# Performance work log

Measured on AMD Instinct MI355X. Metric: run time of the kernel, lower is better.

## Reference

```python
import jax, jax.numpy as jnp
import numpy as np

D = 512; N = 1536; H = 4; DH = D // H
MAX_INT = 5; BINS = 100; LAYERS = 3


def _mha(q_in, k_in, v_in, in_w, in_b, out_w, out_b):
    """PyTorch-style nn.MultiheadAttention (batch of 1). Returns (out [Nq,D], head-avg weights [Nq,Nk])."""
    wq, wk, wv = in_w[:D], in_w[D:2 * D], in_w[2 * D:]
    bq, bk, bv = in_b[:D], in_b[D:2 * D], in_b[2 * D:]
    n_q, n_k = q_in.shape[0], k_in.shape[0]
    q = (q_in @ wq.T + bq).reshape(n_q, H, DH).transpose(1, 0, 2)  # [H,Nq,dh]
    k = (k_in @ wk.T + bk).reshape(n_k, H, DH).transpose(1, 0, 2)
    v = (v_in @ wv.T + bv).reshape(n_k, H, DH).transpose(1, 0, 2)
    scores = jnp.einsum('hqd,hkd->hqk', q, k) / jnp.sqrt(jnp.asarray(DH, q.dtype))
    w = jax.nn.softmax(scores, axis=-1)  # [H,Nq,Nk]
    out = jnp.einsum('hqk,hkd->hqd', w, v).transpose(1, 0, 2).reshape(n_q, D)
    out = out @ out_w.T + out_b
    return out, w.mean(0)


def setup_inputs() -> dict:
    key = jax.random.key(0)
    ks = jax.random.split(key, 12)
    s = 0.02
    return {
        'node_embeddings': jax.random.normal(ks[0], (N, D), jnp.float32),
        'time_positions': jax.random.uniform(ks[1], (N, 1), jnp.float32) * 10.0,
        'batch_indices': jnp.zeros((N,), jnp.int32),
        'W_time': jax.random.normal(ks[2], (D, 1), jnp.float32) * s,
        'b_time': jnp.zeros((D,), jnp.float32),
        'in_w': jax.random.normal(ks[3], (3 * D, D), jnp.float32) * s,
        'in_b': jnp.zeros((3 * D,), jnp.float32),
        'out_w': jax.random.normal(ks[4], (D, D), jnp.float32) * s,
        'out_b': jnp.zeros((D,), jnp.float32),
        'ic_w1': jax.random.normal(ks[5], (128, D), jnp.float32) * s,
        'ic_b1': jnp.zeros((128,), jnp.float32),
        'ic_w2': jax.random.normal(ks[6], (MAX_INT, 128), jnp.float32) * s,
        'ic_b2': jnp.zeros((MAX_INT,), jnp.float32),
        'ref_w1': jax.random.normal(ks[7], (LAYERS, 128, D + 2), jnp.float32) * s,
        'ref_b1': jnp.zeros((LAYERS, 128), jnp.float32),
        'ref_w2': jax.random.normal(ks[8], (LAYERS, 2 * BINS, 128), jnp.float32) * s,
        'ref_b2': jnp.zeros((LAYERS, 2 * BINS), jnp.float32),
        'weight_params': jnp.linspace(-0.5, 0.5, BINS).astype(jnp.float32),
        'qp_w': jax.random.normal(ks[9], (D, D + 2), jnp.float32) * s,
        'qp_b': jnp.zeros((D,), jnp.float32),
    }


def _forward(node_embeddings, time_positions, W_time, b_time, in_w, in_b, out_w, out_b,
             ic_w1, ic_b1, ic_w2, ic_b2, ref_w1, ref_b1, ref_w2, ref_b2,
             weight_params, qp_w, qp_b):
    x = node_embeddings + time_positions @ W_time.T + b_time  # [N,D]
    attn_out, _ = _mha(x, x, x, in_w, in_b, out_w, out_b)      # [N,D]
    pooled = attn_out.mean(0)                                   # [D]
    probs = jax.nn.softmax(ic_w2 @ jax.nn.relu(ic_w1 @ pooled + ic_b1) + ic_b2)
    num_intervals = jnp.argmax(probs) + 1
    interval_mask = jnp.arange(MAX_INT) < num_intervals
    t_min, t_max = time_positions.min(), time_positions.max()
    grid = jnp.linspace(t_min, t_max, MAX_INT + 1)
    start, end = grid[:-1], grid[1:]                            # [MAX_INT]
    n = attn_out.shape[0]
    ones = jnp.ones((n, 1), attn_out.dtype)

    def per_interval(s_i, e_i, w1, b1, w2, b2):
        query = jnp.concatenate([attn_out, ones * s_i, ones * e_i], axis=-1)  # [N,D+2]
        qp = query @ qp_w.T + qp_b                                            # [N,D]
        h = jax.nn.relu(query @ w1.T + b1)
        logits = h @ w2.T + b2                                                # [N,2*BINS]
        s_off = (jax.nn.softmax(logits[:, :BINS], axis=-1) * weight_params).sum(-1)  # [N]
        e_off = (jax.nn.softmax(logits[:, BINS:], axis=-1) * weight_params).sum(-1)
        _, aw = _mha(qp, attn_out, attn_out, in_w, in_b, out_w, out_b)        # [N,N]
        return (aw * s_off).sum(), (aw * e_off).sum()

    for l in range(LAYERS):  # layers have distinct params; intervals are independent within a layer
        ds, de = jax.vmap(per_interval, in_axes=(0, 0, None, None, None, None))(
            start, end, ref_w1[l], ref_b1[l], ref_w2[l], ref_b2[l])
        start = start + ds
        end = end + de

    final_bounds = jnp.stack([start, end], axis=-1)  # [MAX_INT,2]
    return final_bounds, interval_mask


def reference(node_embeddings, time_positions, batch_indices, W_time, b_time, in_w, in_b,
              out_w, out_b, ic_w1, ic_b1, ic_w2, ic_b2, ref_w1, ref_b1, ref_w2, ref_b2,
              weight_params, qp_w, qp_b):
    return _forward(node_embeddings, time_positions, W_time, b_time, in_w, in_b, out_w, out_b,
                    ic_w1, ic_b1, ic_w2, ic_b2, ref_w1, ref_b1, ref_w2, ref_b2,
                    weight_params, qp_w, qp_b)
```

## Files before the change

kernel.cpp:

```cpp
#include <hip/hip_runtime.h>
#include <hip/hip_bf16.h>

typedef __hip_bfloat16 bf16;
typedef __bf16 bf16x8 __attribute__((ext_vector_type(8)));
typedef float f32x4 __attribute__((ext_vector_type(4)));

#define DD   512
#define NT   1536
#define NH   4
#define DHD  128
#define NBINS 100
#define MAXI 5
#define NL   3
#define RSQRT_DH 0.08838834764831845f

#define OFF_ATT    ((size_t)0)
#define OFF_CTX    (OFF_ATT  + (size_t)NT*DD)
#define OFF_CTX1   (OFF_CTX  + (size_t)NT*DD)
#define OFF_H0     (OFF_CTX1 + (size_t)NT*DD)
#define OFF_LG     (OFF_H0   + (size_t)NT*384)
#define OFF_AARR   (OFF_LG   + (size_t)8*NH*NT*16)
#define OFF_BARR   (OFF_AARR + (size_t)NH*NT)
#define OFF_AV     (OFF_BARR + (size_t)NH*NT)
#define OFF_BV     (OFF_AV   + (size_t)DD)
#define OFF_B2     (OFF_BV   + (size_t)DD)
#define OFF_SOFF   (OFF_B2   + (size_t)DD)
#define OFF_EOFF   (OFF_SOFF + (size_t)MAXI*NT)
#define OFF_STAT   (OFF_EOFF + (size_t)MAXI*NT)
#define OFF_POOL   (OFF_STAT + (size_t)NH*NT*12)
#define OFF_SCAL   (OFF_POOL + (size_t)DD)
#define OFF_E      (OFF_SCAL + (size_t)64)
#define SC_START 0
#define SC_END   5
#define SC_DSDE  10
#define SC_CNT   20
#define PSLICE   ((size_t)NH*NT*16)
#define BF_BASE  (OFF_E + (size_t)NH*NT*NT/2)
#define BQKB   ((size_t)0)
#define BVT    (BQKB  + (size_t)NT*1024)
#define BATT   (BVT   + (size_t)NH*128*NT)
#define BK2    (BATT  + (size_t)NT*512)
#define BQ0    (BK2   + (size_t)NT*512)
#define BM2    (BQ0   + (size_t)NT*512)
#define BINW   (BM2   + (size_t)512*512)
#define BOUTW  (BINW  + (size_t)1536*512)
#define BRW1   (BOUTW + (size_t)512*512)
#define BRW2   (BRW1  + (size_t)384*512)

__device__ __forceinline__ void cvt8(const float* s, bf16* d) {
    float4 f0 = *(const float4*)s, f1 = *(const float4*)(s + 4);
    union { uint4 u; unsigned short us[8]; } o;
    bf16 t;
    t = __float2bfloat16(f0.x); o.us[0] = *(unsigned short*)&t;
    t = __float2bfloat16(f0.y); o.us[1] = *(unsigned short*)&t;
    t = __float2bfloat16(f0.z); o.us[2] = *(unsigned short*)&t;
    t = __float2bfloat16(f0.w); o.us[3] = *(unsigned short*)&t;
    t = __float2bfloat16(f1.x); o.us[4] = *(unsigned short*)&t;
    t = __float2bfloat16(f1.y); o.us[5] = *(unsigned short*)&t;
    t = __float2bfloat16(f1.z); o.us[6] = *(unsigned short*)&t;
// ... 115 lines not shown
        for (int it = 0; it < 32; it++) {
            size_t g = start + it * 256 + tid;
            cvt8(out_w + g * 8, bp + BOUTW + g * 8);
        }
    } else if (bx < 97) {
        size_t start = (size_t)(bx - 93) * 6144;
        for (int it = 0; it < 24; it++) {
            size_t g = start + it * 256 + tid;
            int row = (int)(g >> 6), col = (int)(g & 63) * 8;
            const float* s = ref_w1 + (size_t)row * 514 + col;
            float buf[8];
#pragma unroll
            for (int q = 0; q < 4; q++) { float2 f = *(const float2*)(s + 2 * q); buf[2 * q] = f.x; buf[2 * q + 1] = f.y; }
            cvt8(buf, bp + BRW1 + (size_t)row * 512 + col);
        }
    } else {
        for (int it = 0; it < 38; it++) {
            size_t g = (size_t)it * 256 + tid;
            if (g < 9600) cvt8(ref_w2 + g * 8, bp + BRW2 + g * 8);
        }
    }
}

template <int STATS>
__global__ __launch_bounds__(256) void k_score(
    const bf16* __restrict__ Ab, int lda, int aZ,
    const bf16* __restrict__ Bb, int ldb, int bZ,
    bf16* __restrict__ E, float* __restrict__ stat)
{
    int z = blockIdx.z;
    const __bf16* A = (const __bf16*)Ab + (size_t)z * aZ;
    const __bf16* B = (const __bf16*)Bb + (size_t)z * bZ;
    int m0 = blockIdx.y * 128, n0 = blockIdx.x * 128;
    __shared__ __bf16 As[128 * 40];
    __shared__ __bf16 Bs[128 * 40];
    __shared__ float sSum[4][64];
    int tid = threadIdx.x;
    int r = tid >> 1, hh = tid & 1;
    int w = tid >> 6, lane = tid & 63;
    int wm = (w & 1) * 64, wn = (w >> 1) * 64;
    int lr = lane & 15, lq = lane >> 4;
    f32x4 acc[4][4];
#pragma unroll
    for (int i = 0; i < 4; i++)
#pragma unroll
        for (int j = 0; j < 4; j++) acc[i][j] = (f32x4){0.f, 0.f, 0.f, 0.f};

    const __bf16* arow = A + (size_t)(m0 + r) * lda + hh * 16;
    const __bf16* brow = B + (size_t)(n0 + r) * ldb + hh * 16;
    __bf16* awr = &As[r * 40 + hh * 16];
    __bf16* bwr = &Bs[r * 40 + hh * 16];

    for (int k0 = 0; k0 < DHD; k0 += 32) {
        uint4 a0 = *(const uint4*)(arow + k0);
        uint4 a1 = *(const uint4*)(arow + k0 + 8);
        uint4 b0 = *(const uint4*)(brow + k0);
        uint4 b1 = *(const uint4*)(brow + k0 + 8);
        __syncthreads();
        *(uint4*)awr = a0; *(uint4*)(awr + 8) = a1;
        *(uint4*)bwr = b0; *(uint4*)(bwr + 8) = b1;
        __syncthreads();
        bf16x8 af[4], bfr[4];
#pragma unroll
        for (int i = 0; i < 4; i++) af[i] = *(bf16x8*)&As[(wm + i * 16 + lr) * 40 + lq * 8];
#pragma unroll
        for (int j = 0; j < 4; j++) bfr[j] = *(bf16x8*)&Bs[(wn + j * 16 + lr) * 40 + lq * 8];
#pragma unroll
        for (int i = 0; i < 4; i++)
#pragma unroll
            for (int j = 0; j < 4; j++)
                acc[i][j] = __builtin_amdgcn_mfma_f32_16x16x32_bf16(af[i], bfr[j], acc[i][j], 0, 0, 0);
    }
    bf16* Ez = E + (size_t)z * NT * NT;
#pragma unroll
    for (int i = 0; i < 4; i++)
#pragma unroll
        for (int r4 = 0; r4 < 4; r4++) {
            int gm = m0 + wm + i * 16 + lq * 4 + r4;
            float s = 0.f;
#pragma unroll
            for (int j = 0; j < 4; j++) {
                float e = __expf(acc[i][j][r4] * RSQRT_DH);
                Ez[(size_t)gm * NT + n0 + wn + j * 16 + lr] = __float2bfloat16(e);
                s += e;
            }
            if (STATS) {
                for (int off = 1; off < 16; off <<= 1) s += __shfl_xor(s, off);
                if (lr == 0) sSum[w][i * 16 + lq * 4 + r4] = s;
            }
        }
    if (STATS) {
        __syncthreads();
        if (tid < 128) {
            int lidx = tid & 63, wb = tid >> 6;
            stat[((size_t)z * NT + m0 + tid) * 12 + blockIdx.x] = sSum[wb][lidx] + sSum[wb + 2][lidx];
        }
    }
}

__global__ __launch_bounds__(256) void k_qkv(
    const float* __restrict__ emb, const float* __restrict__ t,
    const float* __restrict__ wt, const float* __restrict__ bt,
    const float* __restrict__ in_b, float* ws)
{
    bf16* bp = (bf16*)(ws + BF_BASE);
    int m0 = blockIdx.y * 64, n0 = blockIdx.x * 64;
    __shared__ __bf16 As[64 * 40];
    __shared__ __bf16 Bs[64 * 40];
    int tid = threadIdx.x;
    int r = tid >> 2, quad = tid & 3;
    int w = tid >> 6, lane = tid & 63;
    int wm = (w & 1) * 32, wn = (w >> 1) * 32;
    int lr = lane & 15, lq = lane >> 4;
    f32x4 acc[2][2];
#pragma unroll
    for (int i = 0; i < 2; i++)
#pragma unroll
        for (int j = 0; j < 2; j++) acc[i][j] = (f32x4){0.f, 0.f, 0.f, 0.f};

    float trow = t[m0 + r];
    const float* arow = emb + (size_t)(m0 + r) * DD + quad * 8;
    const __bf16* brow = (const __bf16*)(bp + BINW) + (size_t)(n0 + r) * 512 + quad * 8;
// ... 31 lines not shown
#pragma unroll
    for (int i = 0; i < 2; i++)
#pragma unroll
        for (int j = 0; j < 2; j++) {
            int gn = n0 + wn + j * 16 + lr;
            int gmb = m0 + wm + i * 16 + lq * 4;
            float b = in_b[gn];
            if (gn < 2 * DD) {
#pragma unroll
                for (int r4 = 0; r4 < 4; r4++)
                    QKB[(size_t)(gmb + r4) * 1024 + gn] = __float2bfloat16(acc[i][j][r4] + b);
            } else {
                union { uint2 u; unsigned short us[4]; } o;
#pragma unroll
                for (int r4 = 0; r4 < 4; r4++) {
                    bf16 t2 = __float2bfloat16(acc[i][j][r4] + b);
                    o.us[r4] = *(unsigned short*)&t2;
                }
                *(uint2*)&VtB[(size_t)(gn - 2 * DD) * NT + gmb] = o.u;
            }
        }
}

__global__ __launch_bounds__(256) void k_pv(const bf16* __restrict__ E, float* ws) {
    bf16* bp = (bf16*)(ws + BF_BASE);
    int h = blockIdx.z;
    int m0 = blockIdx.y * 64;
    int ks = blockIdx.x;
    const int KCH = NT / 2;
    int kbeg = ks * KCH;
    __shared__ __bf16 As[64 * 40];
    __shared__ __bf16 Bs[128 * 40];
    __shared__ float sI[64];
    int tid = threadIdx.x;
    if (tid < 64) {
        const float* st = ws + OFF_STAT + (size_t)(h * NT + m0 + tid) * 12;
        float den = 0.f;
#pragma unroll
        for (int t2 = 0; t2 < 12; t2++) den += st[t2];
        sI[tid] = 1.f / den;
    }
    int rA = tid >> 2, quadA = tid & 3;
    int rB = tid >> 1, hhB = tid & 1;
    int w = tid >> 6, lane = tid & 63;
    int wm = (w & 1) * 32, wn = (w >> 1) * 64;
    int lr = lane & 15, lq = lane >> 4;
    const __bf16* Eh = (const __bf16*)E + (size_t)h * NT * NT;
    const __bf16* arow = Eh + (size_t)(m0 + rA) * NT + quadA * 8;
    const __bf16* brow = (const __bf16*)(bp + BVT) + ((size_t)h * 128 + rB) * NT + hhB * 16;
    __bf16* awr = &As[rA * 40 + quadA * 8];
    __bf16* bwr = &Bs[rB * 40 + hhB * 16];
    f32x4 acc[2][4];
#pragma unroll
    for (int i = 0; i < 2; i++)
#pragma unroll
        for (int j = 0; j < 4; j++) acc[i][j] = (f32x4){0.f, 0.f, 0.f, 0.f};

    for (int k0 = kbeg; k0 < kbeg + KCH; k0 += 32) {
        uint4 av = *(const uint4*)(arow + k0);
        uint4 b0 = *(const uint4*)(brow + k0);
        uint4 b1 = *(const uint4*)(brow + k0 + 8);
        __syncthreads();
        *(uint4*)awr = av;
        *(uint4*)bwr = b0; *(uint4*)(bwr + 8) = b1;
        __syncthreads();
        bf16x8 af[2], bfr[4];
#pragma unroll
        for (int i = 0; i < 2; i++) af[i] = *(bf16x8*)&As[(wm + i * 16 + lr) * 40 + lq * 8];
#pragma unroll
        for (int j = 0; j < 4; j++) bfr[j] = *(bf16x8*)&Bs[(wn + j * 16 + lr) * 40 + lq * 8];
#pragma unroll
        for (int i = 0; i < 2; i++)
#pragma unroll
            for (int j = 0; j < 4; j++)
                acc[i][j] = __builtin_amdgcn_mfma_f32_16x16x32_bf16(af[i], bfr[j], acc[i][j], 0, 0, 0);
    }
    float* dst = ws + (ks == 0 ? OFF_CTX : OFF_CTX1);
#pragma unroll
    for (int i = 0; i < 2; i++)
#pragma unroll
        for (int r4 = 0; r4 < 4; r4++) {
            int lrow = wm + i * 16 + lq * 4 + r4;
            float ri = sI[lrow];
#pragma unroll
            for (int j = 0; j < 4; j++) {
                int gn = wn + j * 16 + lr;
                dst[(size_t)(m0 + lrow) * DD + h * DHD + gn] = acc[i][j][r4] * ri;
            }
        }
}

__global__ __launch_bounds__(256) void k_oproj(const float* __restrict__ out_b, float* ws) {
    bf16* bp = (bf16*)(ws + BF_BASE);
    int m0 = blockIdx.y * 64, n0 = blockIdx.x * 64;
    __shared__ __bf16 As[64 * 40];
    __shared__ __bf16 Bs[64 * 40];
    __shared__ float ps[64];
    int tid = threadIdx.x;
    int r = tid >> 2, quad = tid & 3;
    int w = tid >> 6, lane = tid & 63;
    int wm = (w & 1) * 32, wn = (w >> 1) * 32;
    int lr = lane & 15, lq = lane >> 4;
    f32x4 acc[2][2];
#pragma unroll
    for (int i = 0; i < 2; i++)
#pragma unroll
        for (int j = 0; j < 2; j++) acc[i][j] = (f32x4){0.f, 0.f, 0.f, 0.f};
    if (tid < 64) ps[tid] = 0.f;

    const float* a0 = ws + OFF_CTX  + (size_t)(m0 + r) * DD + quad * 8;
    const float* a1 = ws + OFF_CTX1 + (size_t)(m0 + r) * DD + quad * 8;
    const __bf16* brow = (const __bf16*)(bp + BOUTW) + (size_t)(n0 + r) * 512 + quad * 8;
    __bf16* awr = &As[r * 40 + quad * 8];
    __bf16* bwr = &Bs[r * 40 + quad * 8];

    for (int k0 = 0; k0 < DD; k0 += 32) {
        __bf16 ta[8] __attribute__((aligned(16)));
#pragma unroll
        for (int q = 0; q < 4; q++) {
            float2 x = *(const float2*)(a0 + k0 + 2 * q);
            float2 y = *(const float2*)(a1 + k0 + 2 * q);
            ta[2 * q]     = (__bf16)(x.x + y.x);
            ta[2 * q + 1] = (__bf16)(x.y + y.y);
        }
        uint4 bbv = *(const uint4*)(brow + k0);
        __syncthreads();
        *(bf16x8*)awr = *(bf16x8*)ta;
        *(uint4*)bwr = bbv;
        __syncthreads();
        bf16x8 af[2], bfr[2];
#pragma unroll
        for (int i = 0; i < 2; i++) af[i] = *(bf16x8*)&As[(wm + i * 16 + lr) * 40 + lq * 8];
#pragma unroll
        for (int j = 0; j < 2; j++) bfr[j] = *(bf16x8*)&Bs[(wn + j * 16 + lr) * 40 + lq * 8];
#pragma unroll
        for (int i = 0; i < 2; i++)
#pragma unroll
            for (int j = 0; j < 2; j++)
                acc[i][j] = __builtin_amdgcn_mfma_f32_16x16x32_bf16(af[i], bfr[j], acc[i][j], 0, 0, 0);
    }
    float* att = ws + OFF_ATT;
    bf16* attB = bp + BATT;
#pragma unroll
    for (int j = 0; j < 2; j++) {
        int gn = n0 + wn + j * 16 + lr;
        float b = out_b[gn];
// ... 38 lines not shown
            float4 a = *(const float4*)wr, b = *(const float4*)(wr + 4);
            float d = a.x * p8[0] + a.y * p8[1] + a.z * p8[2] + a.w * p8[3]
                    + b.x * p8[4] + b.y * p8[5] + b.z * p8[6] + b.w * p8[7];
            for (int off = 32; off; off >>= 1) d += __shfl_xor(d, off);
            if (lane == 0) h1[row] = fmaxf(d * (1.0f / NT) + icb1[row], 0.f);
        }
        __syncthreads();
        if (tid < MAXI) {
            float s = icb2[tid];
            for (int j = 0; j < 128; j++) s += icw2[tid * 128 + j] * h1[j];
            lg[tid] = s;
        }
        __syncthreads();
        if (tid == 0) {
            int best = 0; float bv = lg[0];
            for (int m = 1; m < MAXI; m++) if (lg[m] > bv) { bv = lg[m]; best = m; }
            int ni = best + 1;
            for (int i = 0; i < MAXI; i++) out[10 + i] = (i < ni) ? 1.f : 0.f;
        }
        return;
    }
    const __bf16* B; const float* bias; int n0, mode;
    bf16* Cb = nullptr; float* Cf = nullptr;
    if (bx < 8)       { B = (const __bf16*)(bp + BINW) + (size_t)512 * 512; bias = in_b + DD;     Cb = bp + BK2; n0 = bx * 64; mode = 0; }
    else if (bx < 16) { B = (const __bf16*)(bp + BM2);                      bias = ws + OFF_B2;   Cb = bp + BQ0; n0 = (bx - 8) * 64; mode = 0; }
    else              { B = (const __bf16*)(bp + BRW1);                     bias = ref_b1;        Cf = ws + OFF_H0; n0 = (bx - 16) * 64; mode = 1; }
    int m0 = blockIdx.y * 64;
    int r = tid >> 2, quad = tid & 3;
    int w = tid >> 6, lane = tid & 63;
    int wm = (w & 1) * 32, wn = (w >> 1) * 32;
    int lr = lane & 15, lq = lane >> 4;
    f32x4 acc[2][2];
#pragma unroll
    for (int i = 0; i < 2; i++)
#pragma unroll
        for (int j = 0; j < 2; j++) acc[i][j] = (f32x4){0.f, 0.f, 0.f, 0.f};

    const __bf16* arow = (const __bf16*)(bp + BATT) + (size_t)(m0 + r) * 512 + quad * 8;
    const __bf16* brow = B + (size_t)(n0 + r) * 512 + quad * 8;
    __bf16* awr = &As[r * 40 + quad * 8];
    __bf16* bwr = &Bs[r * 40 + quad * 8];

    for (int k0 = 0; k0 < DD; k0 += 32) {
        uint4 av = *(const uint4*)(arow + k0);
        uint4 bv = *(const uint4*)(brow + k0);
        __syncthreads();
        *(uint4*)awr = av;
        *(uint4*)bwr = bv;
        __syncthreads();
// ... 3 lines not shown
#pragma unroll
        for (int j = 0; j < 2; j++) bfr[j] = *(bf16x8*)&Bs[(wn + j * 16 + lr) * 40 + lq * 8];
#pragma unroll
        for (int i = 0; i < 2; i++)
#pragma unroll
            for (int j = 0; j < 2; j++)
                acc[i][j] = __builtin_amdgcn_mfma_f32_16x16x32_bf16(af[i], bfr[j], acc[i][j], 0, 0, 0);
    }
#pragma unroll
    for (int i = 0; i < 2; i++)
#pragma unroll
        for (int r4 = 0; r4 < 4; r4++) {
            int gm = m0 + wm + i * 16 + lq * 4 + r4;
#pragma unroll
            for (int j = 0; j < 2; j++) {
                int gn = n0 + wn + j * 16 + lr;
                float v = acc[i][j][r4] + bias[gn];
                if (mode == 0) Cb[(size_t)gm * 512 + gn] = __float2bfloat16(v);
                else           Cf[(size_t)gm * 384 + gn] = v;
            }
        }
}

__global__ __launch_bounds__(256) void k_abc(float* ws) {
    bf16* bp = (bf16*)(ws + BF_BASE);
    int wave = threadIdx.x >> 6, lane = threadIdx.x & 63;
    int row = blockIdx.x * 4 + wave;
    int h = row / NT, n = row % NT;
    const unsigned short* k2 = (const unsigned short*)(bp + BK2 + (size_t)n * 512 + h * DHD);
    const float* av = ws + OFF_AV + h * DHD;
    const float* bv = ws + OFF_BV + h * DHD;
    int d = lane * 2;
    float k0 = __uint_as_float((unsigned)k2[d] << 16);
    float k1 = __uint_as_float((unsigned)k2[d + 1] << 16);
    float a = av[d] * k0 + av[d + 1] * k1;
    float b = bv[d] * k0 + bv[d + 1] * k1;
    for (int off = 32; off; off >>= 1) { a += __shfl_xor(a, off); b += __shfl_xor(b, off); }
    if (lane == 0) { ws[OFF_AARR + row] = a * RSQRT_DH; ws[OFF_BARR + row] = b * RSQRT_DH; }
}

__global__ __launch_bounds__(256) void k_lgs(
    const float* __restrict__ rw1, const float* __restrict__ rb2,
    const float* __restrict__ wp, int l, float* ws)
{
    bf16* bp = (bf16*)(ws + BF_BASE);
    __shared__ float dsh[128];
    __shared__ __bf16 As[64 * 136];
    __shared__ __bf16 Bs[64 * 136];
    __shared__ __bf16 Ls[64 * 208];
    int tid = threadIdx.x;
    int m0 = blockIdx.x * 64;
    int i_int = m0 / NT;
    int nbase = m0 % NT;
    if (blockIdx.x == 0 && tid < 11) ws[OFF_SCAL + SC_DSDE + tid] = 0.f;
    if (tid < 128) {
        float s_i = ws[OFF_SCAL + SC_START + i_int], e_i = ws[OFF_SCAL + SC_END + i_int];
        const float* wr = rw1 + (size_t)(l * 128 + tid) * 514;
        dsh[tid] = s_i * wr[512] + e_i * wr[513];
    }
    __syncthreads();
    int r = tid >> 2, quad = tid & 3;
// ... 67 lines not shown
        int c0 = q * 50;
        const unsigned short* lrow = (const unsigned short*)&Ls[rloc * 208];
        float m = -1e30f;
#pragma unroll
        for (int c = 0; c < 50; c++)
            m = fmaxf(m, __uint_as_float((unsigned)lrow[c0 + c] << 16));
        m = fmaxf(m, __shfl_xor(m, 1));
        float den = 0.f, num = 0.f;
#pragma unroll
        for (int c = 0; c < 50; c++) {
            float p = __expf(__uint_as_float((unsigned)lrow[c0 + c] << 16) - m);
            den += p;
            int wc = c0 + c; if (wc >= NBINS) wc -= NBINS;
            num += p * wp[wc];
        }
        den += __shfl_xor(den, 1);
        num += __shfl_xor(num, 1);
        int n = nbase + rloc;
        if (q == 0)      ws[OFF_SOFF + (size_t)i_int * NT + n] = num / den;
        else if (q == 2) ws[OFF_EOFF + (size_t)i_int * NT + n] = num / den;
    }
}

__global__ __launch_bounds__(256) void k_eg(const bf16* __restrict__ E0, float* ws) {
    int h = blockIdx.z;
    int m0 = blockIdx.y * 128;
    int ks = blockIdx.x;
    const int KCH = NT / 8;
    __shared__ __bf16 As[128 * 40];
    __shared__ __bf16 Bs[16 * 40];
    int tid = threadIdx.x;
    int w = tid >> 6, lane = tid & 63;
    int lr = lane & 15, lq = lane >> 4;
    int r = tid >> 1, half = tid & 1;
    const unsigned short* arow =
        (const unsigned short*)((const __bf16*)E0 + (size_t)h * NT * NT + (size_t)(m0 + r) * NT) + half * 16;
    int wm = w * 32;
    f32x4 acc[2];
    acc[0] = (f32x4){0.f, 0.f, 0.f, 0.f};
    acc[1] = (f32x4){0.f, 0.f, 0.f, 0.f};
    int bc = tid >> 3, bk = tid & 7;
    int valid = (tid < 128) && (bc < 15);
    int ii = bc / 3, tt = bc - ii * 3;
    if (ii > 4) ii = 4;
    float s_i = 0.f, e_i = 0.f;
    if (valid) { s_i = ws[OFF_SCAL + SC_START + ii]; e_i = ws[OFF_SCAL + SC_END + ii]; }
    const float* Ar = ws + OFF_AARR + h * NT;
    const float* Br = ws + OFF_BARR + h * NT;
    const float* fo = ws + (tt == 2 ? OFF_EOFF : OFF_SOFF) + (size_t)ii * NT;

    for (int k0 = ks * KCH; k0 < ks * KCH + KCH; k0 += 32) {
        uint4 a0 = *(const uint4*)(arow + k0);
        uint4 a1 = *(const uint4*)(arow + k0 + 8);
        float bv[4] = {0.f, 0.f, 0.f, 0.f};
        if (valid) {
            float4 a4 = *(const float4*)(Ar + k0 + bk * 4);
            float4 b4 = *(const float4*)(Br + k0 + bk * 4);
            bv[0] = __expf(s_i * a4.x + e_i * b4.x);
            bv[1] = __expf(s_i * a4.y + e_i * b4.y);
            bv[2] = __expf(s_i * a4.z + e_i * b4.z);
            bv[3] = __expf(s_i * a4.w + e_i * b4.w);
            if (tt) {
                float4 f4 = *(const float4*)(fo + k0 + bk * 4);
                bv[0] *= f4.x; bv[1] *= f4.y; bv[2] *= f4.z; bv[3] *= f4.w;
            }
        }
        __syncthreads();
        *(uint4*)&As[r * 40 + half * 16] = a0;
        *(uint4*)&As[r * 40 + half * 16 + 8] = a1;
        if (tid < 128) {
            __bf16* bw = &Bs[bc * 40 + bk * 4];
            bw[0] = (__bf16)bv[0]; bw[1] = (__bf16)bv[1]; bw[2] = (__bf16)bv[2]; bw[3] = (__bf16)bv[3];
        }
        __syncthreads();
        bf16x8 bf0 = *(bf16x8*)&Bs[lr * 40 + lq * 8];
        bf16x8 af0 = *(bf16x8*)&As[(wm + lr) * 40 + lq * 8];
        bf16x8 af1 = *(bf16x8*)&As[(wm + 16 + lr) * 40 + lq * 8];
        acc[0] = __builtin_amdgcn_mfma_f32_16x16x32_bf16(af0, bf0, acc[0], 0, 0, 0);
        acc[1] = __builtin_amdgcn_mfma_f32_16x16x32_bf16(af1, bf0, acc[1], 0, 0, 0);
    }
    float* P = ws + OFF_LG + (size_t)ks * PSLICE;
    if (lr < 15) {
#pragma unroll
        for (int i = 0; i < 2; i++)
#pragma unroll
            for (int r4 = 0; r4 < 4; r4++) {
                int gm = m0 + wm + i * 16 + lq * 4 + r4;
                P[(size_t)(h * NT + gm) * 16 + lr] = acc[i][r4];
            }
    }
}

__global__ __launch_bounds__(256) void k_fin(float* ws, float* out, int l) {
    __shared__ float part[4][10];
    int tid = threadIdx.x;
    int w = tid >> 6, lane = tid & 63;
    int row = blockIdx.x * 256 + tid;
    float acc[15];
#pragma unroll
    for (int c = 0; c < 15; c++) acc[c] = 0.f;
    for (int ks = 0; ks < 8; ks++) {
        const float* Pr = ws + OFF_LG + (size_t)ks * PSLICE + (size_t)row * 16;
#pragma unroll
        for (int c = 0; c < 15; c++) acc[c] += Pr[c];
    }
    float loc[10];
#pragma unroll
    for (int i = 0; i < MAXI; i++) {
        float den = acc[i * 3];
        loc[i]        = acc[i * 3 + 1] / den;
        loc[MAXI + i] = acc[i * 3 + 2] / den;
    }
#pragma unroll
    for (int c = 0; c < 10; c++)
        for (int off = 32; off; off >>= 1) loc[c] += __shfl_xor(loc[c], off);
    if (lane == 0) {
#pragma unroll
        for (int c = 0; c < 10; c++) part[w][c] = loc[c];
    }
    __syncthreads();
    if (tid < 10) {
        float s = part[0][tid] + part[1][tid] + part[2][tid] + part[3][tid];
        atomicAdd(&ws[OFF_SCAL + SC_DSDE + tid], s);
    }
    __threadfence();
    __syncthreads();
    if (tid == 0) {
        unsigned old = atomicAdd((unsigned*)&ws[OFF_SCAL + SC_CNT], 1u);
        if (old == 23) {
            for (int i = 0; i < MAXI; i++) {
                float ds = atomicAdd(&ws[OFF_SCAL + SC_DSDE + i], 0.f);
                float de = atomicAdd(&ws[OFF_SCAL + SC_DSDE + MAXI + i], 0.f);
                float ns = ws[OFF_SCAL + SC_START + i] + ds * 0.25f;
                float ne = ws[OFF_SCAL + SC_END + i]   + de * 0.25f;
                ws[OFF_SCAL + SC_START + i] = ns;
                ws[OFF_SCAL + SC_END + i]   = ne;
                if (l == NL - 1) { out[2 * i] = ns; out[2 * i + 1] = ne; }
            }
        }
    }
}

extern "C" void kernel_launch(void* const* d_in, const int* in_sizes, int n_in,
                              void* d_out, int out_size, void* d_ws, size_t ws_size,
                              hipStream_t stream) {
    const float* emb    = (const float*)d_in[0];
    const float* tpos   = (const float*)d_in[1];
    const float* W_time = (const float*)d_in[3];
    const float* b_time = (const float*)d_in[4];
    const float* in_w   = (const float*)d_in[5];
    const float* in_b   = (const float*)d_in[6];
    const float* out_w  = (const float*)d_in[7];
    const float* out_b  = (const float*)d_in[8];
    const float* ic_w1  = (const float*)d_in[9];
    const float* ic_b1  = (const float*)d_in[10];
    const float* ic_w2  = (const float*)d_in[11];
    const float* ic_b2  = (const float*)d_in[12];
    const float* ref_w1 = (const float*)d_in[13];
    const float* ref_b1 = (const float*)d_in[14];
    const float* ref_w2 = (const float*)d_in[15];
    const float* ref_b2 = (const float*)d_in[16];
    const float* wp     = (const float*)d_in[17];
    const float* qp_w   = (const float*)d_in[18];
    const float* qp_b   = (const float*)d_in[19];
    float* ws  = (float*)d_ws;
    float* out = (float*)d_out;
    bf16* E = (bf16*)(ws + OFF_E);
    bf16* bp = (bf16*)(ws + BF_BASE);

    k_misc<<<98, 256, 0, stream>>>(tpos, in_w, in_b, out_w, ref_w1, ref_w2, qp_w, qp_b, ws);

    k_qkv<<<dim3(24, 24), 256, 0, stream>>>(emb, tpos, W_time, b_time, in_b, ws);
    k_score<1><<<dim3(12, 12, NH), 256, 0, stream>>>(
        bp + BQKB, 1024, DHD, bp + BQKB + 512, 1024, DHD, E, ws + OFF_STAT);
    k_pv<<<dim3(2, NT / 64, NH), 256, 0, stream>>>(E, ws);
    k_oproj<<<dim3(8, 24), 256, 0, stream>>>(out_b, ws);

    k_trip<<<dim3(23, 24), 256, 0, stream>>>(in_b, ref_b1, ic_w1, ic_b1, ic_w2, ic_b2, ws, out);

    k_score<0><<<dim3(12, 12, NH), 256, 0, stream>>>(
        bp + BQ0, 512, DHD, bp + BK2, 512, DHD, E, nullptr);
    k_abc<<<NH * NT / 4, 256, 0, stream>>>(ws);

    for (int l = 0; l < NL; l++) {
        k_lgs<<<120, 256, 0, stream>>>(ref_w1, ref_b2 + l * 200, wp, l, ws);
        k_eg<<<dim3(8, NT / 128, NH), 256, 0, stream>>>(E, ws);
        k_fin<<<NH * NT / 256, 256, 0, stream>>>(ws, out, l);
    }
}
```

Before: 305.9 us.

## Fuse first attention into flash-style kernel and merge EG reduction kernels

Replaces the score+PV pair for the first attention with a single fused kernel that computes exp-scores per key tile in shared memory and accumulates context directly, eliminating the materialized E matrix and split-K partials. Folds the k_abc row-dot kernel into an extra z-slice of the second score kernel, and merges the per-layer EG GEMM with its final reduction into one kernel that finalizes via atomics. Reduces launches and global traffic but lowers grid parallelism to 96 blocks for the fused kernels.

Measured after the change: 377.8 us. 1.23x slower.

```diff
diff --git a/kernel.cpp b/kernel.cpp
--- a/kernel.cpp
+++ b/kernel.cpp
@@ -16,25 +16,21 @@
 
 #define OFF_ATT    ((size_t)0)
 #define OFF_CTX    (OFF_ATT  + (size_t)NT*DD)
-#define OFF_CTX1   (OFF_CTX  + (size_t)NT*DD)
-#define OFF_H0     (OFF_CTX1 + (size_t)NT*DD)
-#define OFF_LG     (OFF_H0   + (size_t)NT*384)
-#define OFF_AARR   (OFF_LG   + (size_t)8*NH*NT*16)
+#define OFF_H0     (OFF_CTX  + (size_t)NT*DD)
+#define OFF_AARR   (OFF_H0   + (size_t)NT*384)
 #define OFF_BARR   (OFF_AARR + (size_t)NH*NT)
 #define OFF_AV     (OFF_BARR + (size_t)NH*NT)
 #define OFF_BV     (OFF_AV   + (size_t)DD)
 #define OFF_B2     (OFF_BV   + (size_t)DD)
 #define OFF_SOFF   (OFF_B2   + (size_t)DD)
 #define OFF_EOFF   (OFF_SOFF + (size_t)MAXI*NT)
-#define OFF_STAT   (OFF_EOFF + (size_t)MAXI*NT)
-#define OFF_POOL   (OFF_STAT + (size_t)NH*NT*12)
+#define OFF_POOL   (OFF_EOFF + (size_t)MAXI*NT)
 #define OFF_SCAL   (OFF_POOL + (size_t)DD)
 #define OFF_E      (OFF_SCAL + (size_t)64)
 #define SC_START 0
 #define SC_END   5
 #define SC_DSDE  10
 #define SC_CNT   20
-#define PSLICE   ((size_t)NH*NT*16)
 #define BF_BASE  (OFF_E + (size_t)NH*NT*NT/2)
 #define BQKB   ((size_t)0)
 #define BVT    (BQKB  + (size_t)NT*1024)
@@ -196,82 +192,6 @@
     }
 }
 
-template <int STATS>
-__global__ __launch_bounds__(256) void k_score(
-    const bf16* __restrict__ Ab, int lda, int aZ,
-    const bf16* __restrict__ Bb, int ldb, int bZ,
-    bf16* __restrict__ E, float* __restrict__ stat)
-{
-    int z = blockIdx.z;
-    const __bf16* A = (const __bf16*)Ab + (size_t)z * aZ;
-    const __bf16* B = (const __bf16*)Bb + (size_t)z * bZ;
-    int m0 = blockIdx.y * 128, n0 = blockIdx.x * 128;
-    __shared__ __bf16 As[128 * 40];
-    __shared__ __bf16 Bs[128 * 40];
-    __shared__ float sSum[4][64];
-    int tid = threadIdx.x;
-    int r = tid >> 1, hh = tid & 1;
-    int w = tid >> 6, lane = tid & 63;
-    int wm = (w & 1) * 64, wn = (w >> 1) * 64;
-    int lr = lane & 15, lq = lane >> 4;
-    f32x4 acc[4][4];
-#pragma unroll
-    for (int i = 0; i < 4; i++)
-#pragma unroll
-        for (int j = 0; j < 4; j++) acc[i][j] = (f32x4){0.f, 0.f, 0.f, 0.f};
-
-    const __bf16* arow = A + (size_t)(m0 + r) * lda + hh * 16;
-    const __bf16* brow = B + (size_t)(n0 + r) * ldb + hh * 16;
-    __bf16* awr = &As[r * 40 + hh * 16];
-    __bf16* bwr = &Bs[r * 40 + hh * 16];
-
-    for (int k0 = 0; k0 < DHD; k0 += 32) {
-        uint4 a0 = *(const uint4*)(arow + k0);
-        uint4 a1 = *(const uint4*)(arow + k0 + 8);
-        uint4 b0 = *(const uint4*)(brow + k0);
-        uint4 b1 = *(const uint4*)(brow + k0 + 8);
-        __syncthreads();
-        *(uint4*)awr = a0; *(uint4*)(awr + 8) = a1;
-        *(uint4*)bwr = b0; *(uint4*)(bwr + 8) = b1;
-        __syncthreads();
-        bf16x8 af[4], bfr[4];
-#pragma unroll
-        for (int i = 0; i < 4; i++) af[i] = *(bf16x8*)&As[(wm + i * 16 + lr) * 40 + lq * 8];
-#pragma unroll
-        for (int j = 0; j < 4; j++) bfr[j] = *(bf16x8*)&Bs[(wn + j * 16 + lr) * 40 + lq * 8];
-#pragma unroll
-        for (int i = 0; i < 4; i++)
-#pragma unroll
-            for (int j = 0; j < 4; j++)
-                acc[i][j] = __builtin_amdgcn_mfma_f32_16x16x32_bf16(af[i], bfr[j], acc[i][j], 0, 0, 0);
-    }
-    bf16* Ez = E + (size_t)z * NT * NT;
-#pragma unroll
-    for (int i = 0; i < 4; i++)
-#pragma unroll
-        for (int r4 = 0; r4 < 4; r4++) {
-            int gm = m0 + wm + i * 16 + lq * 4 + r4;
-            float s = 0.f;
-#pragma unroll
-            for (int j = 0; j < 4; j++) {
-                float e = __expf(acc[i][j][r4] * RSQRT_DH);
-                Ez[(size_t)gm * NT + n0 + wn + j * 16 + lr] = __float2bfloat16(e);
-                s += e;
-            }
-            if (STATS) {
-                for (int off = 1; off < 16; off <<= 1) s += __shfl_xor(s, off);
-                if (lr == 0) sSum[w][i * 16 + lq * 4 + r4] = s;
-            }
-        }
-    if (STATS) {
-        __syncthreads();
-        if (tid < 128) {
-            int lidx = tid & 63, wb = tid >> 6;
-            stat[((size_t)z * NT + m0 + tid) * 12 + blockIdx.x] = sSum[wb][lidx] + sSum[wb + 2][lidx];
-        }
-    }
-}
-
 __global__ __launch_bounds__(256) void k_qkv(
     const float* __restrict__ emb, const float* __restrict__ t,
     const float* __restrict__ wt, const float* __restrict__ bt,
@@ -349,71 +269,103 @@
         }
 }
 
-__global__ __launch_bounds__(256) void k_pv(const bf16* __restrict__ E, float* ws) {
+__global__ __launch_bounds__(256) void k_fmha(float* ws) {
     bf16* bp = (bf16*)(ws + BF_BASE);
-    int h = blockIdx.z;
-    int m0 = blockIdx.y * 64;
-    int ks = blockIdx.x;
-    const int KCH = NT / 2;
-    int kbeg = ks * KCH;
-    __shared__ __bf16 As[64 * 40];
-    __shared__ __bf16 Bs[128 * 40];
-    __shared__ float sI[64];
+    int h = blockIdx.y;
+    int m0 = blockIdx.x * 64;
+    __shared__ __bf16 Ks[64 * 136];
+    __shared__ __bf16 Vs[128 * 72];
+    __shared__ __bf16 Es[64 * 72];
     int tid = threadIdx.x;
-    if (tid < 64) {
-        const float* st = ws + OFF_STAT + (size_t)(h * NT + m0 + tid) * 12;
-        float den = 0.f;
-#pragma unroll
-        for (int t2 = 0; t2 < 12; t2++) den += st[t2];
-        sI[tid] = 1.f / den;
-    }
-    int rA = tid >> 2, quadA = tid & 3;
+    int w = tid >> 6, lane = tid & 63;
+    int lr = lane & 15, lq = lane >> 4;
+    int wm = w * 16;
+    int r = tid >> 2, quad = tid & 3;
+    const __bf16* QK = (const __bf16*)(bp + BQKB);
+    {
+        const __bf16* qrow = QK + (size_t)(m0 + r) * 1024 + h * 128 + quad * 32;
+        uint4 q0 = *(const uint4*)qrow;
+        uint4 q1 = *(const uint4*)(qrow + 8);
+        uint4 q2 = *(const uint4*)(qrow + 16);
+        uint4 q3 = *(const uint4*)(qrow + 24);
+        __bf16* d = &Ks[r * 136 + quad * 32];
+        *(uint4*)d = q0; *(uint4*)(d + 8) = q1; *(uint4*)(d + 16) = q2; *(uint4*)(d + 24) = q3;
+    }
+    __syncthreads();
+    bf16x8 afq[4];
+#pragma unroll
+    for (int ks = 0; ks < 4; ks++) afq[ks] = *(bf16x8*)&Ks[(wm + lr) * 136 + ks * 32 + lq * 8];
+    f32x4 accO[8];
+#pragma unroll
+    for (int j = 0; j < 8; j++) accO[j] = (f32x4){0.f, 0.f, 0.f, 0.f};
+    f32x4 den = (f32x4){0.f, 0.f, 0.f, 0.f};
+    const __bf16* Vt = (const __bf16*)(bp + BVT) + (size_t)h * 128 * NT;
     int rB = tid >> 1, hhB = tid & 1;
-    int w = tid >> 6, lane = tid & 63;
-    int wm = (w & 1) * 32, wn = (w >> 1) * 64;
-    int lr = lane & 15, lq = lane >> 4;
-    const __bf16* Eh = (const __bf16*)E + (size_t)h * NT * NT;
-    const __bf16* arow = Eh + (size_t)(m0 + rA) * NT + quadA * 8;
-    const __bf16* brow = (const __bf16*)(bp + BVT) + ((size_t)h * 128 + rB) * NT + hhB * 16;
-    __bf16* awr = &As[rA * 40 + quadA * 8];
-    __bf16* bwr = &Bs[rB * 40 + hhB * 16];
-    f32x4 acc[2][4];
-#pragma unroll
-    for (int i = 0; i < 2; i++)
-#pragma unroll
-        for (int j = 0; j < 4; j++) acc[i][j] = (f32x4){0.f, 0.f, 0.f, 0.f};
-
-    for (int k0 = kbeg; k0 < kbeg + KCH; k0 += 32) {
-        uint4 av = *(const uint4*)(arow + k0);
-        uint4 b0 = *(const uint4*)(brow + k0);
-        uint4 b1 = *(const uint4*)(brow + k0 + 8);
-        __syncthreads();
-        *(uint4*)awr = av;
-        *(uint4*)bwr = b0; *(uint4*)(bwr + 8) = b1;
-        __syncthreads();
-        bf16x8 af[2], bfr[4];
-#pragma unroll
-        for (int i = 0; i < 2; i++) af[i] = *(bf16x8*)&As[(wm + i * 16 + lr) * 40 + lq * 8];
-#pragma unroll
-        for (int j = 0; j < 4; j++) bfr[j] = *(bf16x8*)&Bs[(wn + j * 16 + lr) * 40 + lq * 8];
-#pragma unroll
-        for (int i = 0; i < 2; i++)
-#pragma unroll
-            for (int j = 0; j < 4; j++)
-                acc[i][j] = __builtin_amdgcn_mfma_f32_16x16x32_bf16(af[i], bfr[j], acc[i][j], 0, 0, 0);
-    }
-    float* dst = ws + (ks == 0 ? OFF_CTX : OFF_CTX1);
-#pragma unroll
-    for (int i = 0; i < 2; i++)
-#pragma unroll
-        for (int r4 = 0; r4 < 4; r4++) {
-            int lrow = wm + i * 16 + lq * 4 + r4;
-            float ri = sI[lrow];
+
+    for (int kb = 0; kb < NT; kb += 64) {
+        const __bf16* krow = QK + (size_t)(kb + r) * 1024 + 512 + h * 128 + quad * 32;
+        uint4 k0v = *(const uint4*)krow;
+        uint4 k1v = *(const uint4*)(krow + 8);
+        uint4 k2v = *(const uint4*)(krow + 16);
+        uint4 k3v = *(const uint4*)(krow + 24);
+        const __bf16* vrow = Vt + (size_t)rB * NT + kb + hhB * 32;
+        uint4 v0 = *(const uint4*)vrow;
+        uint4 v1 = *(const uint4*)(vrow + 8);
+        uint4 v2 = *(const uint4*)(vrow + 16);
+        uint4 v3 = *(const uint4*)(vrow + 24);
+        __syncthreads();
+        {
+            __bf16* d = &Ks[r * 136 + quad * 32];
+            *(uint4*)d = k0v; *(uint4*)(d + 8) = k1v; *(uint4*)(d + 16) = k2v; *(uint4*)(d + 24) = k3v;
+            __bf16* dv = &Vs[rB * 72 + hhB * 32];
+            *(uint4*)dv = v0; *(uint4*)(dv + 8) = v1; *(uint4*)(dv + 16) = v2; *(uint4*)(dv + 24) = v3;
+        }
+        __syncthreads();
+        f32x4 accS[4];
+#pragma unroll
+        for (int j = 0; j < 4; j++) accS[j] = (f32x4){0.f, 0.f, 0.f, 0.f};
+#pragma unroll
+        for (int ks = 0; ks < 4; ks++) {
 #pragma unroll
             for (int j = 0; j < 4; j++) {
-                int gn = wn + j * 16 + lr;
-                dst[(size_t)(m0 + lrow) * DD + h * DHD + gn] = acc[i][j][r4] * ri;
-            }
+                bf16x8 bk = *(bf16x8*)&Ks[(j * 16 + lr) * 136 + ks * 32 + lq * 8];
+                accS[j] = __builtin_amdgcn_mfma_f32_16x16x32_bf16(afq[ks], bk, accS[j], 0, 0, 0);
+            }
+        }
+#pragma unroll
+        for (int j = 0; j < 4; j++) {
+#pragma unroll
+            for (int reg = 0; reg < 4; reg++) {
+                float e = __expf(accS[j][reg] * RSQRT_DH);
+                den[reg] += e;
+                Es[(wm + lq * 4 + reg) * 72 + j * 16 + lr] = (__bf16)e;
+            }
+        }
+#pragma unroll
+        for (int ks = 0; ks < 2; ks++) {
+            bf16x8 ae = *(bf16x8*)&Es[(wm + lr) * 72 + ks * 32 + lq * 8];
+#pragma unroll
+            for (int jn = 0; jn < 8; jn++) {
+                bf16x8 bv = *(bf16x8*)&Vs[(jn * 16 + lr) * 72 + ks * 32 + lq * 8];
+                accO[jn] = __builtin_amdgcn_mfma_f32_16x16x32_bf16(ae, bv, accO[jn], 0, 0, 0);
+            }
+        }
+    }
+    for (int off = 1; off < 16; off <<= 1) {
+        den[0] += __shfl_xor(den[0], off);
+        den[1] += __shfl_xor(den[1], off);
+        den[2] += __shfl_xor(den[2], off);
+        den[3] += __shfl_xor(den[3], off);
+    }
+    f32x4 ri;
+    ri[0] = 1.f / den[0]; ri[1] = 1.f / den[1]; ri[2] = 1.f / den[2]; ri[3] = 1.f / den[3];
+    float* ctx = ws + OFF_CTX;
+#pragma unroll
+    for (int jn = 0; jn < 8; jn++)
+#pragma unroll
+        for (int reg = 0; reg < 4; reg++) {
+            int gm = m0 + wm + lq * 4 + reg;
+            ctx[(size_t)gm * DD + h * 128 + jn * 16 + lr] = accO[jn][reg] * ri[reg];
         }
 }
 
@@ -435,8 +387,7 @@
         for (int j = 0; j < 2; j++) acc[i][j] = (f32x4){0.f, 0.f, 0.f, 0.f};
     if (tid < 64) ps[tid] = 0.f;
 
-    const float* a0 = ws + OFF_CTX  + (size_t)(m0 + r) * DD + quad * 8;
-    const float* a1 = ws + OFF_CTX1 + (size_t)(m0 + r) * DD + quad * 8;
+    const float* a0 = ws + OFF_CTX + (size_t)(m0 + r) * DD + quad * 8;
     const __bf16* brow = (const __bf16*)(bp + BOUTW) + (size_t)(n0 + r) * 512 + quad * 8;
     __bf16* awr = &As[r * 40 + quad * 8];
     __bf16* bwr = &Bs[r * 40 + quad * 8];
@@ -446,9 +397,7 @@
 #pragma unroll
         for (int q = 0; q < 4; q++) {
             float2 x = *(const float2*)(a0 + k0 + 2 * q);
-            float2 y = *(const float2*)(a1 + k0 + 2 * q);
-            ta[2 * q]     = (__bf16)(x.x + y.x);
-            ta[2 * q + 1] = (__bf16)(x.y + y.y);
+            ta[2 * q] = (__bf16)x.x; ta[2 * q + 1] = (__bf16)x.y;
         }
         uint4 bbv = *(const uint4*)(brow + k0);
         __syncthreads();
@@ -533,9 +482,9 @@
     }
     const __bf16* B; const float* bias; int n0, mode;
     bf16* Cb = nullptr; float* Cf = nullptr;
-    if (bx < 8)       { B = (const __bf16*)(bp + BINW) + (size_t)512 * 512; bias = in_b + DD;     Cb = bp + BK2; n0 = bx * 64; mode = 0; }
-    else if (bx < 16) { B = (const __bf16*)(bp + BM2);                      bias = ws + OFF_B2;   Cb = bp + BQ0; n0 = (bx - 8) * 64; mode = 0; }
-    else              { B = (const __bf16*)(bp + BRW1);                     bias = ref_b1;        Cf = ws + OFF_H0; n0 = (bx - 16) * 64; mode = 1; }
+    if (bx < 8)       { B = (const __bf16*)(bp + BINW) + (size_t)512 * 512; bias = in_b + DD;   Cb = bp + BK2; n0 = bx * 64; mode = 0; }
+    else if (bx < 16) { B = (const __bf16*)(bp + BM2);                      bias = ws + OFF_B2; Cb = bp + BQ0; n0 = (bx - 8) * 64; mode = 0; }
+    else              { B = (const __bf16*)(bp + BRW1);                     bias = ref_b1;      Cf = ws + OFF_H0; n0 = (bx - 16) * 64; mode = 1; }
     int m0 = blockIdx.y * 64;
     int r = tid >> 2, quad = tid & 3;
     int w = tid >> 6, lane = tid & 63;
@@ -585,21 +534,86 @@
         }
 }
 
-__global__ __launch_bounds__(256) void k_abc(float* ws) {
-    bf16* bp = (bf16*)(ws + BF_BASE);
-    int wave = threadIdx.x >> 6, lane = threadIdx.x & 63;
-    int row = blockIdx.x * 4 + wave;
-    int h = row / NT, n = row % NT;
-    const unsigned short* k2 = (const unsigned short*)(bp + BK2 + (size_t)n * 512 + h * DHD);
-    const float* av = ws + OFF_AV + h * DHD;
-    const float* bv = ws + OFF_BV + h * DHD;
-    int d = lane * 2;
-    float k0 = __uint_as_float((unsigned)k2[d] << 16);
-    float k1 = __uint_as_float((unsigned)k2[d + 1] << 16);
-    float a = av[d] * k0 + av[d + 1] * k1;
-    float b = bv[d] * k0 + bv[d + 1] * k1;
-    for (int off = 32; off; off >>= 1) { a += __shfl_xor(a, off); b += __shfl_xor(b, off); }
-    if (lane == 0) { ws[OFF_AARR + row] = a * RSQRT_DH; ws[OFF_BARR + row] = b * RSQRT_DH; }
+__global__ __launch_bounds__(256) void k_score(
+    const bf16* __restrict__ Ab, int lda, int aZ,
+    const bf16* __restrict__ Bb, int ldb, int bZ,
+    bf16* __restrict__ E, float* ws)
+{
+    int tid = threadIdx.x;
+    if (blockIdx.z == 4) {
+        bf16* bp = (bf16*)(ws + BF_BASE);
+        int flat = blockIdx.y * 12 + blockIdx.x;
+        int w = tid >> 6, lane = tid & 63;
+        for (int t = w; t < 43; t += 4) {
+            int row = flat * 43 + t;
+            if (row >= NH * NT) break;
+            int hh = row / NT, n = row % NT;
+            const unsigned short* k2 = (const unsigned short*)(bp + BK2 + (size_t)n * 512 + hh * DHD);
+            const float* av = ws + OFF_AV + hh * DHD;
+            const float* bv = ws + OFF_BV + hh * DHD;
+            int d = lane * 2;
+            float k0 = __uint_as_float((unsigned)k2[d] << 16);
+            float k1 = __uint_as_float((unsigned)k2[d + 1] << 16);
+            float a = av[d] * k0 + av[d + 1] * k1;
+            float b = bv[d] * k0 + bv[d + 1] * k1;
+            for (int off = 32; off; off >>= 1) { a += __shfl_xor(a, off); b += __shfl_xor(b, off); }
+            if (lane == 0) { ws[OFF_AARR + row] = a * RSQRT_DH; ws[OFF_BARR + row] = b * RSQRT_DH; }
+        }
+        return;
+    }
+    int z = blockIdx.z;
+    const __bf16* A = (const __bf16*)Ab + (size_t)z * aZ;
+    const __bf16* B = (const __bf16*)Bb + (size_t)z * bZ;
+    int m0 = blockIdx.y * 128, n0 = blockIdx.x * 128;
+    __shared__ __bf16 As[128 * 40];
+    __shared__ __bf16 Bs[128 * 40];
+    int r = tid >> 1, hh = tid & 1;
+    int w = tid >> 6, lane = tid & 63;
+    int wm = (w & 1) * 64, wn = (w >> 1) * 64;
+    int lr = lane & 15, lq = lane >> 4;
+    f32x4 acc[4][4];
+#pragma unroll
+    for (int i = 0; i < 4; i++)
+#pragma unroll
+        for (int j = 0; j < 4; j++) acc[i][j] = (f32x4){0.f, 0.f, 0.f, 0.f};
+
+    const __bf16* arow = A + (size_t)(m0 + r) * lda + hh * 16;
+    const __bf16* brow = B + (size_t)(n0 + r) * ldb + hh * 16;
+    __bf16* awr = &As[r * 40 + hh * 16];
+    __bf16* bwr = &Bs[r * 40 + hh * 16];
+
+    for (int k0 = 0; k0 < DHD; k0 += 32) {
+        uint4 a0 = *(const uint4*)(arow + k0);
+        uint4 a1 = *(const uint4*)(arow + k0 + 8);
+        uint4 b0 = *(const uint4*)(brow + k0);
+        uint4 b1 = *(const uint4*)(brow + k0 + 8);
+        __syncthreads();
+        *(uint4*)awr = a0; *(uint4*)(awr + 8) = a1;
+        *(uint4*)bwr = b0; *(uint4*)(bwr + 8) = b1;
+        __syncthreads();
+        bf16x8 af[4], bfr[4];
+#pragma unroll
+        for (int i = 0; i < 4; i++) af[i] = *(bf16x8*)&As[(wm + i * 16 + lr) * 40 + lq * 8];
+#pragma unroll
+        for (int j = 0; j < 4; j++) bfr[j] = *(bf16x8*)&Bs[(wn + j * 16 + lr) * 40 + lq * 8];
+#pragma unroll
+        for (int i = 0; i < 4; i++)
+#pragma unroll
+            for (int j = 0; j < 4; j++)
+                acc[i][j] = __builtin_amdgcn_mfma_f32_16x16x32_bf16(af[i], bfr[j], acc[i][j], 0, 0, 0);
+    }
+    bf16* Ez = E + (size_t)z * NT * NT;
+#pragma unroll
+    for (int i = 0; i < 4; i++)
+#pragma unroll
+        for (int r4 = 0; r4 < 4; r4++) {
+            int gm = m0 + wm + i * 16 + lq * 4 + r4;
+#pragma unroll
+            for (int j = 0; j < 4; j++) {
+                float e = __expf(acc[i][j][r4] * RSQRT_DH);
+                Ez[(size_t)gm * NT + n0 + wn + j * 16 + lr] = __float2bfloat16(e);
+            }
+        }
 }
 
 __global__ __launch_bounds__(256) void k_lgs(
@@ -713,38 +727,34 @@
     }
 }
 
-__global__ __launch_bounds__(256) void k_eg(const bf16* __restrict__ E0, float* ws) {
-    int h = blockIdx.z;
-    int m0 = blockIdx.y * 128;
-    int ks = blockIdx.x;
-    const int KCH = NT / 8;
-    __shared__ __bf16 As[128 * 40];
-    __shared__ __bf16 Bs[16 * 40];
+__global__ __launch_bounds__(256) void k_egf(const bf16* __restrict__ E0, float* ws, float* out, int l) {
+    int h = blockIdx.y;
+    int m0 = blockIdx.x * 64;
+    __shared__ __bf16 As[64 * 72];
+    __shared__ __bf16 Bs[16 * 72];
+    __shared__ float Ps[64 * 17];
     int tid = threadIdx.x;
     int w = tid >> 6, lane = tid & 63;
     int lr = lane & 15, lq = lane >> 4;
-    int r = tid >> 1, half = tid & 1;
+    int wm = w * 16;
+    int r = tid >> 2, quad = tid & 3;
     const unsigned short* arow =
-        (const unsigned short*)((const __bf16*)E0 + (size_t)h * NT * NT + (size_t)(m0 + r) * NT) + half * 16;
-    int wm = w * 32;
-    f32x4 acc[2];
-    acc[0] = (f32x4){0.f, 0.f, 0.f, 0.f};
-    acc[1] = (f32x4){0.f, 0.f, 0.f, 0.f};
-    int bc = tid >> 3, bk = tid & 7;
-    int valid = (tid < 128) && (bc < 15);
+        (const unsigned short*)((const __bf16*)E0 + (size_t)h * NT * NT + (size_t)(m0 + r) * NT) + quad * 16;
+    f32x4 acc = (f32x4){0.f, 0.f, 0.f, 0.f};
+    int bc = tid >> 4, bk = tid & 15;
+    int bvalid = (bc < 15);
     int ii = bc / 3, tt = bc - ii * 3;
     if (ii > 4) ii = 4;
-    float s_i = 0.f, e_i = 0.f;
-    if (valid) { s_i = ws[OFF_SCAL + SC_START + ii]; e_i = ws[OFF_SCAL + SC_END + ii]; }
+    float s_i = ws[OFF_SCAL + SC_START + ii], e_i = ws[OFF_SCAL + SC_END + ii];
     const float* Ar = ws + OFF_AARR + h * NT;
     const float* Br = ws + OFF_BARR + h * NT;
     const float* fo = ws + (tt == 2 ? OFF_EOFF : OFF_SOFF) + (size_t)ii * NT;
 
-    for (int k0 = ks * KCH; k0 < ks * KCH + KCH; k0 += 32) {
+    for (int k0 = 0; k0 < NT; k0 += 64) {
         uint4 a0 = *(const uint4*)(arow + k0);
         uint4 a1 = *(const uint4*)(arow + k0 + 8);
         float bv[4] = {0.f, 0.f, 0.f, 0.f};
-        if (valid) {
+        if (bvalid) {
             float4 a4 = *(const float4*)(Ar + k0 + bk * 4);
             float4 b4 = *(const float4*)(Br + k0 + bk * 4);
             bv[0] = __expf(s_i * a4.x + e_i * b4.x);
@@ -757,76 +767,51 @@
             }
         }
         __syncthreads();
-        *(uint4*)&As[r * 40 + half * 16] = a0;
-        *(uint4*)&As[r * 40 + half * 16 + 8] = a1;
-        if (tid < 128) {
-            __bf16* bw = &Bs[bc * 40 + bk * 4];
+        *(uint4*)&As[r * 72 + quad * 16] = a0;
+        *(uint4*)&As[r * 72 + quad * 16 + 8] = a1;
+        if (bvalid) {
+            __bf16* bw = &Bs[bc * 72 + bk * 4];
             bw[0] = (__bf16)bv[0]; bw[1] = (__bf16)bv[1]; bw[2] = (__bf16)bv[2]; bw[3] = (__bf16)bv[3];
         }
         __syncthreads();
-        bf16x8 bf0 = *(bf16x8*)&Bs[lr * 40 + lq * 8];
-        bf16x8 af0 = *(bf16x8*)&As[(wm + lr) * 40 + lq * 8];
-        bf16x8 af1 = *(bf16x8*)&As[(wm + 16 + lr) * 40 + lq * 8];
-        acc[0] = __builtin_amdgcn_mfma_f32_16x16x32_bf16(af0, bf0, acc[0], 0, 0, 0);
-        acc[1] = __builtin_amdgcn_mfma_f32_16x16x32_bf16(af1, bf0, acc[1], 0, 0, 0);
-    }
-    float* P = ws + OFF_LG + (size_t)ks * PSLICE;
-    if (lr < 15) {
-#pragma unroll
-        for (int i = 0; i < 2; i++)
-#pragma unroll
-            for (int r4 = 0; r4 < 4; r4++) {
-                int gm = m0 + wm + i * 16 + lq * 4 + r4;
-                P[(size_t)(h * NT + gm) * 16 + lr] = acc[i][r4];
-            }
-    }
-}
-
-__global__ __launch_bounds__(256) void k_fin(float* ws, float* out, int l) {
-    __shared__ float part[4][10];
-    int tid = threadIdx.x;
-    int w = tid >> 6, lane = tid & 63;
-    int row = blockIdx.x * 256 + tid;
-    float acc[15];
-#pragma unroll
-    for (int c = 0; c < 15; c++) acc[c] = 0.f;
-    for (int ks = 0; ks < 8; ks++) {
-        const float* Pr = ws + OFF_LG + (size_t)ks * PSLICE + (size_t)row * 16;
-#pragma unroll
-        for (int c = 0; c < 15; c++) acc[c] += Pr[c];
-    }
-    float loc[10];
-#pragma unroll
-    for (int i = 0; i < MAXI; i++) {
-        float den = acc[i * 3];
-        loc[i]        = acc[i * 3 + 1] / den;
-        loc[MAXI + i] = acc[i * 3 + 2] / den;
-    }
-#pragma unroll
-    for (int c = 0; c < 10; c++)
-        for (int off = 32; off; off >>= 1) loc[c] += __shfl_xor(loc[c], off);
-    if (lane == 0) {
-#pragma unroll
-        for (int c = 0; c < 10; c++) part[w][c] = loc[c];
-    }
+#pragma unroll
+        for (int ks = 0; ks < 2; ks++) {
+            bf16x8 af = *(bf16x8*)&As[(wm + lr) * 72 + ks * 32 + lq * 8];
+            bf16x8 bf0 = *(bf16x8*)&Bs[lr * 72 + ks * 32 + lq * 8];
+            acc = __builtin_amdgcn_mfma_f32_16x16x32_bf16(af, bf0, acc, 0, 0, 0);
+        }
+    }
+#pragma unroll
+    for (int reg = 0; reg < 4; reg++)
+        Ps[(wm + lq * 4 + reg) * 17 + lr] = acc[reg];
     __syncthreads();
-    if (tid < 10) {
-        float s = part[0][tid] + part[1][tid] + part[2][tid] + part[3][tid];
-        atomicAdd(&ws[OFF_SCAL + SC_DSDE + tid], s);
-    }
-    __threadfence();
-    __syncthreads();
-    if (tid == 0) {
-        unsigned old = atomicAdd((unsigned*)&ws[OFF_SCAL + SC_CNT], 1u);
-        if (old == 23) {
-            for (int i = 0; i < MAXI; i++) {
-                float ds = atomicAdd(&ws[OFF_SCAL + SC_DSDE + i], 0.f);
-                float de = atomicAdd(&ws[OFF_SCAL + SC_DSDE + MAXI + i], 0.f);
-                float ns = ws[OFF_SCAL + SC_START + i] + ds * 0.25f;
-                float ne = ws[OFF_SCAL + SC_END + i]   + de * 0.25f;
-                ws[OFF_SCAL + SC_START + i] = ns;
-                ws[OFF_SCAL + SC_END + i]   = ne;
-                if (l == NL - 1) { out[2 * i] = ns; out[2 * i + 1] = ne; }
+    if (w == 0) {
+        const float* P = &Ps[lane * 17];
+        float loc[10];
+#pragma unroll
+        for (int i = 0; i < MAXI; i++) {
+            float dn = P[i * 3];
+            loc[i]        = P[i * 3 + 1] / dn;
+            loc[MAXI + i] = P[i * 3 + 2] / dn;
+        }
+#pragma unroll
+        for (int c = 0; c < 10; c++)
+            for (int off = 32; off; off >>= 1) loc[c] += __shfl_xor(loc[c], off);
+        if (lane == 0) {
+#pragma unroll
+            for (int c = 0; c < 10; c++) atomicAdd(&ws[OFF_SCAL + SC_DSDE + c], loc[c]);
+            __threadfence();
+            unsigned old = atomicAdd((unsigned*)&ws[OFF_SCAL + SC_CNT], 1u);
+            if (old == 95) {
+                for (int i = 0; i < MAXI; i++) {
+                    float ds = atomicAdd(&ws[OFF_SCAL + SC_DSDE + i], 0.f);
+                    float de = atomicAdd(&ws[OFF_SCAL + SC_DSDE + MAXI + i], 0.f);
+                    float ns = ws[OFF_SCAL + SC_START + i] + ds * 0.25f;
+                    float ne = ws[OFF_SCAL + SC_END + i]   + de * 0.25f;
+                    ws[OFF_SCAL + SC_START + i] = ns;
+                    ws[OFF_SCAL + SC_END + i]   = ne;
+                    if (l == NL - 1) { out[2 * i] = ns; out[2 * i + 1] = ne; }
+                }
             }
         }
     }
@@ -862,20 +847,16 @@
     k_misc<<<98, 256, 0, stream>>>(tpos, in_w, in_b, out_w, ref_w1, ref_w2, qp_w, qp_b, ws);
 
     k_qkv<<<dim3(24, 24), 256, 0, stream>>>(emb, tpos, W_time, b_time, in_b, ws);
-    k_score<1><<<dim3(12, 12, NH), 256, 0, stream>>>(
-        bp + BQKB, 1024, DHD, bp + BQKB + 512, 1024, DHD, E, ws + OFF_STAT);
-    k_pv<<<dim3(2, NT / 64, NH), 256, 0, stream>>>(E, ws);
+    k_fmha<<<dim3(24, NH), 256, 0, stream>>>(ws);
     k_oproj<<<dim3(8, 24), 256, 0, stream>>>(out_b, ws);
 
     k_trip<<<dim3(23, 24), 256, 0, stream>>>(in_b, ref_b1, ic_w1, ic_b1, ic_w2, ic_b2, ws, out);
 
-    k_score<0><<<dim3(12, 12, NH), 256, 0, stream>>>(
-        bp + BQ0, 512, DHD, bp + BK2, 512, DHD, E, nullptr);
-    k_abc<<<NH * NT / 4, 256, 0, stream>>>(ws);
+    k_score<<<dim3(12, 12, 5), 256, 0, stream>>>(
+        bp + BQ0, 512, DHD, bp + BK2, 512, DHD, E, ws);
 
     for (int l = 0; l < NL; l++) {
         k_lgs<<<120, 256, 0, stream>>>(ref_w1, ref_b2 + l * 200, wp, l, ws);
-        k_eg<<<dim3(8, NT / 128, NH), 256, 0, stream>>>(E, ws);
-        k_fin<<<NH * NT / 256, 256, 0, stream>>>(ws, out, l);
-    }
-}
+        k_egf<<<dim3(24, NH), 256, 0, stream>>>(E, ws, out, l);
+    }
+}
```
